# Performance work log

Hardware: AMD Instinct MI355X
Metric: run time of the kernel (lower is better)

The kernel has to match this reference:

```python
import jax, jax.numpy as jnp
import numpy as np

N_NODES = 100000
N_EDGES = 1600000
D_FEAT = 64
LATENT = 64
N_CLASSES = 16
NEG_SLOPE = 0.01  # flax nn.leaky_relu default negative_slope


def setup_inputs() -> dict:
    key = jax.random.key(0)
    ks = jax.random.split(key, 5)
    nodes = jax.random.normal(ks[0], (N_NODES, D_FEAT), dtype=jnp.float32)
    senders = jax.random.randint(ks[1], (N_EDGES,), 0, N_NODES)
    receivers = jax.random.randint(ks[2], (N_EDGES,), 0, N_NODES)
    # learned params (flax Dense: y = x @ kernel + bias)
    W0 = jax.random.normal(ks[3], (D_FEAT, LATENT), dtype=jnp.float32) / jnp.sqrt(D_FEAT)
    b0 = jnp.zeros((LATENT,), jnp.float32)
    W1 = jax.random.normal(ks[4], (LATENT, N_CLASSES), dtype=jnp.float32) / jnp.sqrt(LATENT)
    b1 = jnp.zeros((N_CLASSES,), jnp.float32)
    return {"nodes": nodes, "senders": senders, "receivers": receivers,
            "W0": W0, "b0": b0, "W1": W1, "b1": b1}


def _gcn_forward(nodes, W0, b0, W1, b1, senders, receivers):
    n = nodes.shape[0]
    ones = jnp.ones_like(senders, dtype=nodes.dtype)
    deg_s = jax.ops.segment_sum(ones, senders, n)    # out-degree of each node as sender
    deg_r = jax.ops.segment_sum(ones, receivers, n)  # in-degree of each node as receiver

    # Layer 1: GraphConvolution(Dense(latent), symmetric_normalization=True)
    h = nodes @ W0 + b0                                                  # [N, latent]
    h = h * jax.lax.rsqrt(jnp.maximum(deg_s, 1.0))[:, None]
    h = jax.ops.segment_sum(h[senders], receivers, n)                    # gather-scatter over edges
    h = h * jax.lax.rsqrt(jnp.maximum(deg_r, 1.0))[:, None]
    h = jnp.where(h >= 0, h, NEG_SLOPE * h)                              # leaky_relu

    # Layer 2: GraphConvolution(Dense(classes)+sigmoid, symmetric_normalization=False)
    z = jax.nn.sigmoid(h @ W1 + b1)                                      # [N, classes]
    out = jax.ops.segment_sum(z[senders], receivers, n)                  # unnormalized aggregation
    return out


def reference(nodes, senders, receivers, W0, b0, W1, b1):
    return _gcn_forward(nodes, W0, b0, W1, b1, senders, receivers)
```

## Files before the change

kernel.cpp:

```cpp
#include <hip/hip_runtime.h>
#include <hip/hip_bf16.h>

#define NN 100000
#define NE 1600000
#define D 64
#define C 16
#define NEG_SLOPE 0.01f
#define MCAP 64

#define NXCD 8
#define RNG 12500
#define NSL 782
#define EPSL 2048
#define B_BUILD (NSL * NXCD)

#define NRANGE 8
#define RW 12544
#define WPR 3136
#define NSLICE 64
#define EPS 25000
#define B_HIST (NRANGE * NSLICE)

#define B_GEMM 6250

typedef unsigned int u32;
typedef unsigned short u16;

__device__ __forceinline__ float bf2f(u32 u) { return __uint_as_float(u << 16); }
__device__ __forceinline__ u16 f2bf(float f) {
    __hip_bfloat16 b = __float2bfloat16(f);
    return *reinterpret_cast<u16*>(&b);
}

__global__ __launch_bounds__(256) void kA(
        const int* __restrict__ senders, const int* __restrict__ receivers,
        const float* __restrict__ nodes, const float* __restrict__ W0,
        const float* __restrict__ b0,
        int* __restrict__ cnt_r, int* __restrict__ bucket,
        u16* __restrict__ h, u32* __restrict__ part) {
    __shared__ u32 smh[WPR];
    int bid = blockIdx.x, t = threadIdx.x;

    if (bid < B_BUILD) {
        int slice = bid >> 3, range = bid & 7;
        int lo = range * RNG;
        int e0 = slice * EPSL;
#pragma unroll
        for (int k = 0; k < 8; ++k) {
            int e = e0 + k * 256 + t;
            if (e < NE) {
                int r = receivers[e];
                if ((u32)(r - lo) < (u32)RNG) {
                    int s = senders[e];
                    int slot = atomicAdd(&cnt_r[r], 1);
                    if (slot < MCAP) bucket[r * MCAP + slot] = s;
                }
            }
        }
    } else if (bid < B_BUILD + B_GEMM) {
        int wv = (bid - B_BUILD) * 4 + (t >> 6);
        int lane = t & 63;
        int nsub = lane >> 4, q = lane & 15;
        int node = wv * 4 + nsub;
        const float* __restrict__ row = nodes + (size_t)node * D;
        float4 acc = ((const float4*)b0)[q];
#pragma unroll 16
        for (int k = 0; k < D; ++k) {
            float rk = row[k];
            float4 w4 = ((const float4*)(W0 + k * D))[q];
            acc.x = fmaf(rk, w4.x, acc.x);
            acc.y = fmaf(rk, w4.y, acc.y);
            acc.z = fmaf(rk, w4.z, acc.z);
            acc.w = fmaf(rk, w4.w, acc.w);
        }
        uint2 pk;
        pk.x = (u32)f2bf(acc.x) | ((u32)f2bf(acc.y) << 16);
        pk.y = (u32)f2bf(acc.z) | ((u32)f2bf(acc.w) << 16);
        *(uint2*)(h + (size_t)node * D + q * 4) = pk;
    } else {
        int hb = bid - B_BUILD - B_GEMM;
        int rr = hb & 7, sl = hb >> 3;
        int lo = rr * RW;
        for (int i = t; i < WPR; i += 256) smh[i] = 0u;
        __syncthreads();
        const int* __restrict__ sp = senders + sl * EPS;
        for (int i = t; i < EPS; i += 256) {
            int local = sp[i] - lo;
            if ((u32)local < (u32)RW)
                atomicAdd(&smh[local >> 2], 1u << ((local & 3) * 8));
        }
        __syncthreads();
        u32* __restrict__ dst = part + (size_t)hb * WPR;
        for (int i = t; i < WPR; i += 256) dst[i] = smh[i];
    }
}

__global__ __launch_bounds__(256) void k0b(const u32* __restrict__ part,
                                           float* __restrict__ rnorm_s) {
    int tid = blockIdx.x * 256 + threadIdx.x;
    int rr = tid / WPR;
    int w = tid - rr * WPR;
    const u32* __restrict__ p = part + (size_t)rr * WPR + w;
    u32 acc0 = 0, acc1 = 0;
#pragma unroll 8
    for (int sl = 0; sl < NSLICE; ++sl) {
        u32 v = p[(size_t)(sl * 8) * WPR];
        acc0 += v & 0x00FF00FFu;
        acc1 += (v >> 8) & 0x00FF00FFu;
    }
    int node = rr * RW + w * 4;
    u32 c0 = acc0 & 0xFFFFu, c1 = acc1 & 0xFFFFu, c2 = acc0 >> 16, c3 = acc1 >> 16;
    if (node + 3 < NN) {
        float4 o;
        o.x = rsqrtf((float)(c0 > 1u ? c0 : 1u));
        o.y = rsqrtf((float)(c1 > 1u ? c1 : 1u));
        o.z = rsqrtf((float)(c2 > 1u ? c2 : 1u));
        o.w = rsqrtf((float)(c3 > 1u ? c3 : 1u));
        *(float4*)(rnorm_s + node) = o;
    } else {
        u32 cc[4] = {c0, c1, c2, c3};
        for (int k = 0; k < 4; ++k)
            if (node + k < NN)
                rnorm_s[node + k] = rsqrtf((float)(cc[k] > 1u ? cc[k] : 1u));
    }
}

__global__ __launch_bounds__(256) void kB(
        const int* __restrict__ cnt_r, const int* __restrict__ bucket,
        const float* __restrict__ rnorm_s, const u16* __restrict__ h,
        const float* __restrict__ W1, const float* __restrict__ b1,
        u16* __restrict__ z) {
    __shared__ float sm[4][64];
    int wid = threadIdx.x >> 6, lane = threadIdx.x & 63;
    int node = blockIdx.x * 4 + wid;
    int deg = cnt_r[node];
    if (deg > MCAP) deg = MCAP;
    const int* __restrict__ row = bucket + node * MCAP;

    int my = 0; float rq = 0.f;
    if (lane < deg) {
        my = row[lane];
        rq = rnorm_s[my];
    }
    int qtr = lane >> 4, ql = lane & 15;
    float a0 = 0.f, a1 = 0.f, a2 = 0.f, a3 = 0.f;
    for (int j = 0; j < deg; j += 4) {
        int ei = j + qtr;
        int src = __shfl(my, ei, 64);
        float rs = __shfl(rq, ei, 64);
        uint2 w2 = *(const uint2*)(h + (size_t)src * D + ql * 4);
        if (ei < deg) {
            a0 = fmaf(rs, bf2f(w2.x & 0xffffu), a0);
            a1 = fmaf(rs, bf2f(w2.x >> 16),     a1);
            a2 = fmaf(rs, bf2f(w2.y & 0xffffu), a2);
            a3 = fmaf(rs, bf2f(w2.y >> 16),     a3);
        }
    }
    a0 += __shfl_xor(a0, 16, 64); a0 += __shfl_xor(a0, 32, 64);
    a1 += __shfl_xor(a1, 16, 64); a1 += __shfl_xor(a1, 32, 64);
    a2 += __shfl_xor(a2, 16, 64); a2 += __shfl_xor(a2, 32, 64);
    a3 += __shfl_xor(a3, 16, 64); a3 += __shfl_xor(a3, 32, 64);
    if (qtr == 0) {
        float rn = rsqrtf((float)(deg > 1 ? deg : 1));
        float v0 = a0 * rn; v0 = (v0 >= 0.f) ? v0 : NEG_SLOPE * v0;
        float v1 = a1 * rn; v1 = (v1 >= 0.f) ? v1 : NEG_SLOPE * v1;
        float v2 = a2 * rn; v2 = (v2 >= 0.f) ? v2 : NEG_SLOPE * v2;
        float v3 = a3 * rn; v3 = (v3 >= 0.f) ? v3 : NEG_SLOPE * v3;
        sm[wid][ql * 4 + 0] = v0;
        sm[wid][ql * 4 + 1] = v1;
        sm[wid][ql * 4 + 2] = v2;
        sm[wid][ql * 4 + 3] = v3;
    }
    __syncthreads();

    int c = lane & 15, q = lane >> 4;
    float p = 0.f;
#pragma unroll
    for (int i = 0; i < 16; ++i)
        p = fmaf(sm[wid][q * 16 + i], W1[(q * 16 + i) * C + c], p);
    p += __shfl_xor(p, 16, 64);
    p += __shfl_xor(p, 32, 64);
    if (lane < 16) {
        float zc = 1.f / (1.f + expf(-(p + b1[c])));
        z[(size_t)node * C + c] = f2bf(zc);
    }
}

__global__ __launch_bounds__(256) void kC(
        const int* __restrict__ cnt_r, const int* __restrict__ bucket,
        const u16* __restrict__ z, float* __restrict__ out) {
    int idx = blockIdx.x * 256 + threadIdx.x;
    int node = idx >> 6;
    int lane = threadIdx.x & 63;
    int deg = cnt_r[node];
    if (deg > MCAP) deg = MCAP;
    const int* __restrict__ row = bucket + node * MCAP;

    int my = (lane < deg) ? row[lane] : 0;
    int g = lane >> 2, p = lane & 3;
    float a0 = 0.f, a1 = 0.f, a2 = 0.f, a3 = 0.f;
    for (int j = 0; j < deg; j += 16) {
        int ei = j + g;
        int src = __shfl(my, ei, 64);
        uint2 w2 = *(const uint2*)(z + (size_t)src * C + p * 4);
        if (ei < deg) {
            a0 += bf2f(w2.x & 0xffffu);
            a1 += bf2f(w2.x >> 16);
            a2 += bf2f(w2.y & 0xffffu);
            a3 += bf2f(w2.y >> 16);
        }
    }
    a0 += __shfl_xor(a0, 4, 64); a0 += __shfl_xor(a0, 8, 64);
    a0 += __shfl_xor(a0, 16, 64); a0 += __shfl_xor(a0, 32, 64);
    a1 += __shfl_xor(a1, 4, 64); a1 += __shfl_xor(a1, 8, 64);
    a1 += __shfl_xor(a1, 16, 64); a1 += __shfl_xor(a1, 32, 64);
    a2 += __shfl_xor(a2, 4, 64); a2 += __shfl_xor(a2, 8, 64);
    a2 += __shfl_xor(a2, 16, 64); a2 += __shfl_xor(a2, 32, 64);
    a3 += __shfl_xor(a3, 4, 64); a3 += __shfl_xor(a3, 8, 64);
    a3 += __shfl_xor(a3, 16, 64); a3 += __shfl_xor(a3, 32, 64);
    if (lane < 4) {
        float4 o; o.x = a0; o.y = a1; o.z = a2; o.w = a3;
        *(float4*)(out + (size_t)node * C + p * 4) = o;
    }
}

extern "C" void kernel_launch(void* const* d_in, const int* in_sizes, int n_in,
                              void* d_out, int out_size, void* d_ws, size_t ws_size,
                              hipStream_t stream) {
    const float* nodes     = (const float*)d_in[0];
    const int*   senders   = (const int*)d_in[1];
    const int*   receivers = (const int*)d_in[2];
    const float* W0        = (const float*)d_in[3];
    const float* b0        = (const float*)d_in[4];
    const float* W1        = (const float*)d_in[5];
    const float* b1        = (const float*)d_in[6];
    float* out = (float*)d_out;

    char* wsb = (char*)d_ws;
    int*   cnt_r   = (int*)wsb;
    u32*   part    = (u32*)(wsb + 400000);
    float* rnorm_s = (float*)(wsb + 6822528);
    int*   bucket  = (int*)(wsb + 7222528);
    u16*   h       = (u16*)(wsb + 32822528);
    u16*   z       = (u16*)(wsb + 45622528);

    hipMemsetAsync(cnt_r, 0, NN * sizeof(int), stream);

    kA<<<B_BUILD + B_GEMM + B_HIST, 256, 0, stream>>>(senders, receivers, nodes, W0, b0,
                                                      cnt_r, bucket, h, part);
    k0b<<<98, 256, 0, stream>>>(part, rnorm_s);
    kB<<<25000, 256, 0, stream>>>(cnt_r, bucket, rnorm_s, h, W1, b1, z);
    kC<<<25000, 256, 0, stream>>>(cnt_r, bucket, z, out);
}
```

Baseline: 326.4 us.

## Build receiver buckets via LDS histogram, prefix scan, then fill pass

Replaces the global-atomic bucket build (one atomicAdd on cnt_r per edge) with a two-pass approach. First, per-slice LDS histograms of receivers are computed. Then an exclusive scan over slices produces per-slice offsets and the final counts. A fill kernel then places senders using LDS atomics plus those offsets. This removes the memset and global atomic contention, but adds an extra kernel, a second read of the edges, and only 128 fill blocks, which may limit parallelism.

```diff
diff --git a/kernel.cpp b/kernel.cpp
--- a/kernel.cpp
+++ b/kernel.cpp
@@ -10,16 +10,17 @@
 
 #define NXCD 8
 #define RNG 12500
-#define NSL 782
-#define EPSL 2048
-#define B_BUILD (NSL * NXCD)
+#define HWORDS 6250
+#define NS 16
+#define EPSL 100000
+#define B_HR (NS * NXCD)
 
 #define NRANGE 8
 #define RW 12544
 #define WPR 3136
 #define NSLICE 64
 #define EPS 25000
-#define B_HIST (NRANGE * NSLICE)
+#define B_HS (NRANGE * NSLICE)
 
 #define B_GEMM 6250
 
@@ -36,29 +37,41 @@
         const int* __restrict__ senders, const int* __restrict__ receivers,
         const float* __restrict__ nodes, const float* __restrict__ W0,
         const float* __restrict__ b0,
-        int* __restrict__ cnt_r, int* __restrict__ bucket,
-        u16* __restrict__ h, u32* __restrict__ part) {
-    __shared__ u32 smh[WPR];
+        u32* __restrict__ part_r, u32* __restrict__ part_s, u16* __restrict__ h) {
+    __shared__ u32 smh[HWORDS];
     int bid = blockIdx.x, t = threadIdx.x;
 
-    if (bid < B_BUILD) {
+    if (bid < B_HR) {
         int slice = bid >> 3, range = bid & 7;
         int lo = range * RNG;
-        int e0 = slice * EPSL;
-#pragma unroll
-        for (int k = 0; k < 8; ++k) {
-            int e = e0 + k * 256 + t;
-            if (e < NE) {
-                int r = receivers[e];
-                if ((u32)(r - lo) < (u32)RNG) {
-                    int s = senders[e];
-                    int slot = atomicAdd(&cnt_r[r], 1);
-                    if (slot < MCAP) bucket[r * MCAP + slot] = s;
-                }
-            }
-        }
-    } else if (bid < B_BUILD + B_GEMM) {
-        int wv = (bid - B_BUILD) * 4 + (t >> 6);
+        for (int i = t; i < HWORDS; i += 256) smh[i] = 0u;
+        __syncthreads();
+        const int* __restrict__ rp = receivers + slice * EPSL;
+        for (int i = t; i < EPSL; i += 256) {
+            int rl = rp[i] - lo;
+            if ((u32)rl < (u32)RNG)
+                atomicAdd(&smh[rl >> 1], 1u << ((rl & 1) * 16));
+        }
+        __syncthreads();
+        u32* __restrict__ dst = part_r + ((size_t)slice * NXCD + range) * HWORDS;
+        for (int i = t; i < HWORDS; i += 256) dst[i] = smh[i];
+    } else if (bid < B_HR + B_HS) {
+        int hb = bid - B_HR;
+        int rr = hb & 7, sl = hb >> 3;
+        int lo = rr * RW;
+        for (int i = t; i < WPR; i += 256) smh[i] = 0u;
+        __syncthreads();
+        const int* __restrict__ sp = senders + sl * EPS;
+        for (int i = t; i < EPS; i += 256) {
+            int local = sp[i] - lo;
+            if ((u32)local < (u32)RW)
+                atomicAdd(&smh[local >> 2], 1u << ((local & 3) * 8));
+        }
+        __syncthreads();
+        u32* __restrict__ dst = part_s + (size_t)hb * WPR;
+        for (int i = t; i < WPR; i += 256) dst[i] = smh[i];
+    } else {
+        int wv = (bid - B_HR - B_HS) * 4 + (t >> 6);
         int lane = t & 63;
         int nsub = lane >> 4, q = lane & 15;
         int node = wv * 4 + nsub;
@@ -77,51 +90,89 @@
         pk.x = (u32)f2bf(acc.x) | ((u32)f2bf(acc.y) << 16);
         pk.y = (u32)f2bf(acc.z) | ((u32)f2bf(acc.w) << 16);
         *(uint2*)(h + (size_t)node * D + q * 4) = pk;
+    }
+}
+
+__global__ __launch_bounds__(256) void kSc(u32* __restrict__ part_r,
+                                           const u32* __restrict__ part_s,
+                                           int* __restrict__ cnt_r,
+                                           float* __restrict__ rnorm_s) {
+    int bid = blockIdx.x, t = threadIdx.x;
+    if (bid < 196) {
+        int tid = bid * 256 + t;
+        if (tid < NXCD * HWORDS) {
+            int range = tid / HWORDS, w = tid - range * HWORDS;
+            u32* __restrict__ base = part_r + (size_t)range * HWORDS + w;
+            u32 s0 = 0, s1 = 0;
+#pragma unroll
+            for (int sl = 0; sl < NS; ++sl) {
+                u32* p = base + (size_t)sl * (NXCD * HWORDS);
+                u32 v = *p;
+                *p = s0 | (s1 << 16);
+                s0 += v & 0xffffu;
+                s1 += v >> 16;
+            }
+            int node = range * RNG + 2 * w;
+            cnt_r[node] = (int)s0;
+            cnt_r[node + 1] = (int)s1;
+        }
     } else {
-        int hb = bid - B_BUILD - B_GEMM;
-        int rr = hb & 7, sl = hb >> 3;
-        int lo = rr * RW;
-        for (int i = t; i < WPR; i += 256) smh[i] = 0u;
-        __syncthreads();
-        const int* __restrict__ sp = senders + sl * EPS;
-        for (int i = t; i < EPS; i += 256) {
-            int local = sp[i] - lo;
-            if ((u32)local < (u32)RW)
-                atomicAdd(&smh[local >> 2], 1u << ((local & 3) * 8));
-        }
-        __syncthreads();
-        u32* __restrict__ dst = part + (size_t)hb * WPR;
-        for (int i = t; i < WPR; i += 256) dst[i] = smh[i];
-    }
-}
-
-__global__ __launch_bounds__(256) void k0b(const u32* __restrict__ part,
-                                           float* __restrict__ rnorm_s) {
-    int tid = blockIdx.x * 256 + threadIdx.x;
-    int rr = tid / WPR;
-    int w = tid - rr * WPR;
-    const u32* __restrict__ p = part + (size_t)rr * WPR + w;
-    u32 acc0 = 0, acc1 = 0;
+        int tid = (bid - 196) * 256 + t;
+        if (tid < NRANGE * WPR) {
+            int rr = tid / WPR;
+            int w = tid - rr * WPR;
+            const u32* __restrict__ p = part_s + (size_t)rr * WPR + w;
+            u32 acc0 = 0, acc1 = 0;
 #pragma unroll 8
-    for (int sl = 0; sl < NSLICE; ++sl) {
-        u32 v = p[(size_t)(sl * 8) * WPR];
-        acc0 += v & 0x00FF00FFu;
-        acc1 += (v >> 8) & 0x00FF00FFu;
-    }
-    int node = rr * RW + w * 4;
-    u32 c0 = acc0 & 0xFFFFu, c1 = acc1 & 0xFFFFu, c2 = acc0 >> 16, c3 = acc1 >> 16;
-    if (node + 3 < NN) {
-        float4 o;
-        o.x = rsqrtf((float)(c0 > 1u ? c0 : 1u));
-        o.y = rsqrtf((float)(c1 > 1u ? c1 : 1u));
-        o.z = rsqrtf((float)(c2 > 1u ? c2 : 1u));
-        o.w = rsqrtf((float)(c3 > 1u ? c3 : 1u));
-        *(float4*)(rnorm_s + node) = o;
-    } else {
-        u32 cc[4] = {c0, c1, c2, c3};
-        for (int k = 0; k < 4; ++k)
-            if (node + k < NN)
-                rnorm_s[node + k] = rsqrtf((float)(cc[k] > 1u ? cc[k] : 1u));
+            for (int sl = 0; sl < NSLICE; ++sl) {
+                u32 v = p[(size_t)(sl * 8) * WPR];
+                acc0 += v & 0x00FF00FFu;
+                acc1 += (v >> 8) & 0x00FF00FFu;
+            }
+            int node = rr * RW + w * 4;
+            u32 c0 = acc0 & 0xFFFFu, c1 = acc1 & 0xFFFFu, c2 = acc0 >> 16, c3 = acc1 >> 16;
+            if (node + 3 < NN) {
+                float4 o;
+                o.x = rsqrtf((float)(c0 > 1u ? c0 : 1u));
+                o.y = rsqrtf((float)(c1 > 1u ? c1 : 1u));
+                o.z = rsqrtf((float)(c2 > 1u ? c2 : 1u));
+                o.w = rsqrtf((float)(c3 > 1u ? c3 : 1u));
+                *(float4*)(rnorm_s + node) = o;
+            } else {
+                u32 cc[4] = {c0, c1, c2, c3};
+                for (int k = 0; k < 4; ++k)
+                    if (node + k < NN)
+                        rnorm_s[node + k] = rsqrtf((float)(cc[k] > 1u ? cc[k] : 1u));
+            }
+        }
+    }
+}
+
+__global__ __launch_bounds__(256) void kF(
+        const int* __restrict__ senders, const int* __restrict__ receivers,
+        const u32* __restrict__ part_r,
+        int* __restrict__ bucket) {
+    __shared__ u32 smh[HWORDS];
+    int bid = blockIdx.x, t = threadIdx.x;
+    int slice = bid >> 3, range = bid & 7;
+    int lo = range * RNG;
+    for (int i = t; i < HWORDS; i += 256) smh[i] = 0u;
+    __syncthreads();
+    const u32* __restrict__ pre = part_r + ((size_t)slice * NXCD + range) * HWORDS;
+    int e0 = slice * EPSL;
+    for (int i = t; i < EPSL; i += 256) {
+        int e = e0 + i;
+        int rl = receivers[e] - lo;
+        if ((u32)rl < (u32)RNG) {
+            int s = senders[e];
+            int w = rl >> 1, sh = (rl & 1) * 16;
+            u32 old = atomicAdd(&smh[w], 1u << sh);
+            u32 local = (old >> sh) & 0xffffu;
+            u32 base = (pre[w] >> sh) & 0xffffu;
+            int slot = (int)(base + local);
+            if (slot < MCAP)
+                bucket[(lo + rl) * MCAP + slot] = s;
+        }
     }
 }
 
@@ -237,18 +288,18 @@
     float* out = (float*)d_out;
 
     char* wsb = (char*)d_ws;
-    int*   cnt_r   = (int*)wsb;
-    u32*   part    = (u32*)(wsb + 400000);
-    float* rnorm_s = (float*)(wsb + 6822528);
-    int*   bucket  = (int*)(wsb + 7222528);
-    u16*   h       = (u16*)(wsb + 32822528);
-    u16*   z       = (u16*)(wsb + 45622528);
-
-    hipMemsetAsync(cnt_r, 0, NN * sizeof(int), stream);
-
-    kA<<<B_BUILD + B_GEMM + B_HIST, 256, 0, stream>>>(senders, receivers, nodes, W0, b0,
-                                                      cnt_r, bucket, h, part);
-    k0b<<<98, 256, 0, stream>>>(part, rnorm_s);
+    u32*   part_r  = (u32*)wsb;
+    u32*   part_s  = (u32*)(wsb + 3200000);
+    int*   cnt_r   = (int*)(wsb + 9622528);
+    float* rnorm_s = (float*)(wsb + 10022528);
+    int*   bucket  = (int*)(wsb + 10422528);
+    u16*   h       = (u16*)(wsb + 36022528);
+    u16*   z       = (u16*)(wsb + 48822528);
+
+    kA<<<B_HR + B_HS + B_GEMM, 256, 0, stream>>>(senders, receivers, nodes, W0, b0,
+                                                 part_r, part_s, h);
+    kSc<<<294, 256, 0, stream>>>(part_r, part_s, cnt_r, rnorm_s);
+    kF<<<B_HR, 256, 0, stream>>>(senders, receivers, part_r, bucket);
     kB<<<25000, 256, 0, stream>>>(cnt_r, bucket, rnorm_s, h, W1, b1, z);
     kC<<<25000, 256, 0, stream>>>(cnt_r, bucket, z, out);
 }
```

Result: slower. 621.6 us (+90.5%).
